# Kernel optimization log

Measured on AMD Instinct MI355X. Metric: run time of the kernel, lower is better.

## Reference

```python
import jax, jax.numpy as jnp
import numpy as np

B, N, D, S = 4, 8, 64, 8192  # batch, heads, dim_head, seq_len


def setup_inputs() -> dict:
    key = jax.random.key(0)
    kq, kk, kv = jax.random.split(key, 3)
    q = jax.random.normal(kq, (B, N, D, S), dtype=jnp.float32)
    k = jax.random.normal(kk, (B, N, D, S), dtype=jnp.float32)
    v = jax.random.normal(kv, (B, N, D, S), dtype=jnp.float32)
    return {"q": q, "k": k, "v": v}


def reference(q, k, v):
    # q, k, v: [b, n, d, s] = [batch, heads, dim_head, seq]
    scale = q.shape[-2] ** -0.5  # dim_head^-0.5
    qs = jax.nn.softmax(q, axis=-2) * scale   # softmax over feature dim
    ks = jax.nn.softmax(k, axis=-1)           # softmax over seq dim
    # kv context: [b, n, d, d] -- avoids the O(s^2) score matrix
    context = jnp.einsum('bnis,bnjs->bnij', ks, v)
    # out: [b, n, d, s]
    return jnp.einsum('bnij,bnis->bnjs', context, qs)
```

## Files before the change

kernel.cpp:

```cpp
#include <hip/hip_runtime.h>
#include <math.h>


constexpr int BHEADS = 32;
constexpr int DH     = 64;
constexpr int SEQ    = 8192;
constexpr float QSCALE = 0.125f;

__global__ __launch_bounds__(256)
void ctx_kernel(const float* __restrict__ K, const float* __restrict__ V,
                float* __restrict__ ctx, float* __restrict__ Z)
{
    const int head  = blockIdx.y;
    const int chunk = blockIdx.x;
    const int t     = threadIdx.x;

    const float* kh = K + (size_t)head * DH * SEQ;
    const float* vh = V + (size_t)head * DH * SEQ;

    __shared__ __align__(16) float et[64 * 64];
    __shared__ __align__(16) float vt[64 * 64];

    const int ti  = t >> 4;
    const int tj  = t & 15;
    const int s_l = t & 63;
    const int g   = t >> 6;

    float acc[4][4];
    #pragma unroll
    for (int a = 0; a < 4; ++a)
        #pragma unroll
        for (int b = 0; b < 4; ++b) acc[a][b] = 0.0f;
    float zacc[4] = {0.f, 0.f, 0.f, 0.f};

    for (int st = 0; st < 4; ++st) {
        const int s_base = chunk * 256 + st * 64;
        #pragma unroll
        for (int p = 0; p < 4; ++p) {
            const int c  = g + 4 * p;
            const int i0 = 4 * c;
            const size_t col = (size_t)s_base + s_l;
            float4 e4, v4;
            e4.x = __expf(kh[(size_t)(i0 + 0) * SEQ + col]);
            e4.y = __expf(kh[(size_t)(i0 + 1) * SEQ + col]);
            e4.z = __expf(kh[(size_t)(i0 + 2) * SEQ + col]);
            e4.w = __expf(kh[(size_t)(i0 + 3) * SEQ + col]);
            v4.x = vh[(size_t)(i0 + 0) * SEQ + col];
            v4.y = vh[(size_t)(i0 + 1) * SEQ + col];
            v4.z = vh[(size_t)(i0 + 2) * SEQ + col];
            v4.w = vh[(size_t)(i0 + 3) * SEQ + col];
            const int pos = c ^ (s_l & 15);
            ((float4*)(et + s_l * 64))[pos] = e4;
            ((float4*)(vt + s_l * 64))[pos] = v4;
        }
        __syncthreads();
        #pragma unroll 4
        for (int s = 0; s < 64; ++s) {
            const float4 e4 = ((const float4*)(et + s * 64))[ti ^ (s & 15)];
            const float4 v4 = ((const float4*)(vt + s * 64))[tj ^ (s & 15)];
            const float ee[4] = {e4.x, e4.y, e4.z, e4.w};
            const float vv[4] = {v4.x, v4.y, v4.z, v4.w};
            #pragma unroll
            for (int a = 0; a < 4; ++a) {
                #pragma unroll
                for (int b = 0; b < 4; ++b)
                    acc[a][b] = fmaf(ee[a], vv[b], acc[a][b]);
            }
            zacc[0] += ee[0]; zacc[1] += ee[1];
            zacc[2] += ee[2]; zacc[3] += ee[3];
        }
        __syncthreads();
    }

    float* ch = ctx + head * DH * DH;
    #pragma unroll
    for (int a = 0; a < 4; ++a)
        #pragma unroll
        for (int b = 0; b < 4; ++b)
            unsafeAtomicAdd(&ch[(4 * ti + a) * DH + 4 * tj + b], acc[a][b]);
    if (tj == 0) {
        #pragma unroll
        for (int a = 0; a < 4; ++a)
            unsafeAtomicAdd(&Z[head * DH + 4 * ti + a], zacc[a]);
    }
}

__global__ __launch_bounds__(256)
void out_kernel(const float* __restrict__ Q, const float* __restrict__ ctx,
                const float* __restrict__ Z, float* __restrict__ out)
{
    const int head  = blockIdx.y;
    const int stile = blockIdx.x;
    const int t     = threadIdx.x;
    const int s0    = stile * 128;

    __shared__ __align__(16) float eq[64 * 128];
    __shared__ __align__(16) float cs[64 * 64];
    __shared__ float rz[64];
    __shared__ float wpart[2][128];
    __shared__ __align__(16) float wsh[128];

    const float* qh = Q + (size_t)head * DH * SEQ + s0;

    if (t < 64) rz[t] = 1.0f / Z[head * DH + t];

    {
        const int i  = t >> 4;
        const int sg = t & 15;
        #pragma unroll
        for (int p = 0; p < 4; ++p) {
            const int row = i + 16 * p;
            #pragma unroll
            for (int h = 0; h < 2; ++h) {
                const int col = 4 * sg + 64 * h;
                float4 qv = *(const float4*)(qh + (size_t)row * SEQ + col);
                float4 ev;
                ev.x = __expf(qv.x); ev.y = __expf(qv.y);
                ev.z = __expf(qv.z); ev.w = __expf(qv.w);
                *(float4*)(eq + row * 128 + col) = ev;
            }
        }
    }
    __syncthreads();

    {
        const int i  = t >> 2;
        const int jg = t & 3;
        const float* ch = ctx + head * DH * DH;
        const float r = rz[i];
        #pragma unroll
        for (int p = 0; p < 4; ++p) {
            const int j0 = 4 * (jg + 4 * p);
            float4 cv = *(const float4*)(ch + i * DH + j0);
            cv.x *= r; cv.y *= r; cv.z *= r; cv.w *= r;
            *(float4*)(cs + i * DH + j0) = cv;
        }
    }
    {
        const int s = t & 127;
        const int h = t >> 7;
        float w = 0.0f;
        #pragma unroll 8
        for (int i = 32 * h; i < 32 * h + 32; ++i) w += eq[i * 128 + s];
        wpart[h][s] = w;
    }
    __syncthreads();
    if (t < 128) wsh[t] = QSCALE / (wpart[0][t] + wpart[1][t]);
    __syncthreads();

    const int tj = t >> 4;
    const int ts = t & 15;
    float acca[4][4], accb[4][4];
    #pragma unroll
    for (int a = 0; a < 4; ++a)
        #pragma unroll
        for (int b = 0; b < 4; ++b) { acca[a][b] = 0.f; accb[a][b] = 0.f; }

    #pragma unroll 4
    for (int i = 0; i < 64; ++i) {
        const float4 c4 = *(const float4*)(cs + i * DH + 4 * tj);
        const float4 a4 = *(const float4*)(eq + i * 128 + 4 * ts);
        const float4 b4 = *(const float4*)(eq + i * 128 + 64 + 4 * ts);
        const float cc[4] = {c4.x, c4.y, c4.z, c4.w};
        const float aa[4] = {a4.x, a4.y, a4.z, a4.w};
        const float bb[4] = {b4.x, b4.y, b4.z, b4.w};
        #pragma unroll
        for (int j = 0; j < 4; ++j) {
            #pragma unroll
            for (int x = 0; x < 4; ++x) {
                acca[j][x] = fmaf(cc[j], aa[x], acca[j][x]);
                accb[j][x] = fmaf(cc[j], bb[x], accb[j][x]);
            }
        }
    }

    const float4 wa = *(const float4*)(wsh + 4 * ts);
    const float4 wb = *(const float4*)(wsh + 64 + 4 * ts);
    float* oh = out + (size_t)head * DH * SEQ + s0;
    #pragma unroll
    for (int j = 0; j < 4; ++j) {
        const int row = 4 * tj + j;
        float4 o1, o2;
        o1.x = acca[j][0] * wa.x; o1.y = acca[j][1] * wa.y;
        o1.z = acca[j][2] * wa.z; o1.w = acca[j][3] * wa.w;
        o2.x = accb[j][0] * wb.x; o2.y = accb[j][1] * wb.y;
        o2.z = accb[j][2] * wb.z; o2.w = accb[j][3] * wb.w;
        *(float4*)(oh + (size_t)row * SEQ + 4 * ts) = o1;
        *(float4*)(oh + (size_t)row * SEQ + 64 + 4 * ts) = o2;
    }
}

extern "C" void kernel_launch(void* const* d_in, const int* in_sizes, int n_in,
                              void* d_out, int out_size, void* d_ws, size_t ws_size,
                              hipStream_t stream)
{
    const float* q = (const float*)d_in[0];
    const float* k = (const float*)d_in[1];
    const float* v = (const float*)d_in[2];
    float* out = (float*)d_out;

    float* ctx = (float*)d_ws;
    float* Z   = ctx + BHEADS * DH * DH;

    const size_t zero_bytes = (size_t)(BHEADS * DH * DH + BHEADS * DH) * sizeof(float);
    hipMemsetAsync(d_ws, 0, zero_bytes, stream);

    ctx_kernel<<<dim3(32, BHEADS), 256, 0, stream>>>(k, v, ctx, Z);
    out_kernel<<<dim3(64, BHEADS), 256, 0, stream>>>(q, ctx, Z, out);
}
```

Measured before the change: 272.4 us.

## Use fp16 MFMA for both context and output GEMMs with register prefetch

Both kernels replace their scalar FP32 FMA outer-product loops with 16x16x32 fp16 MFMA instructions. Exponentiated K, V, Q and the normalised context are converted to half precision in LDS. Global loads become float4 and are prefetched into registers for the next 64-column tile, overlapping memory with compute. The output kernel now handles 256 sequence columns per block in four sub-tiles with half the grid, and Z is reduced through shared memory before the atomics. The fp16 conversion trades accuracy for throughput, so exp values and V in half precision may lose precision.

```diff
diff --git a/kernel.cpp b/kernel.cpp
--- a/kernel.cpp
+++ b/kernel.cpp
@@ -1,6 +1,10 @@
 #include <hip/hip_runtime.h>
 #include <math.h>
 
+
+typedef _Float16 half8 __attribute__((ext_vector_type(8)));
+typedef _Float16 half4v __attribute__((ext_vector_type(4)));
+typedef float floatx4 __attribute__((ext_vector_type(4)));
 
 constexpr int BHEADS = 32;
 constexpr int DH     = 64;
@@ -14,74 +18,87 @@
     const int head  = blockIdx.y;
     const int chunk = blockIdx.x;
     const int t     = threadIdx.x;
+    const int lane  = t & 63;
+    const int w     = t >> 6;
+    const int ln    = lane & 15;
+    const int q8    = lane >> 4;
 
     const float* kh = K + (size_t)head * DH * SEQ;
     const float* vh = V + (size_t)head * DH * SEQ;
 
-    __shared__ __align__(16) float et[64 * 64];
-    __shared__ __align__(16) float vt[64 * 64];
-
-    const int ti  = t >> 4;
-    const int tj  = t & 15;
-    const int s_l = t & 63;
-    const int g   = t >> 6;
-
-    float acc[4][4];
-    #pragma unroll
-    for (int a = 0; a < 4; ++a)
-        #pragma unroll
-        for (int b = 0; b < 4; ++b) acc[a][b] = 0.0f;
+    __shared__ __align__(16) _Float16 et[64 * 72];
+    __shared__ __align__(16) _Float16 vt[64 * 72];
+    __shared__ float zred[64 * 16];
+
+    const int r0 = t >> 4;
+    const int sc = 4 * (t & 15);
+    const int s_blk = chunk * 256;
+
+    float4 pk[4], pv[4];
+    #pragma unroll
+    for (int p = 0; p < 4; ++p) {
+        const size_t off = (size_t)(r0 + 16 * p) * SEQ + s_blk + sc;
+        pk[p] = *(const float4*)(kh + off);
+        pv[p] = *(const float4*)(vh + off);
+    }
+
+    floatx4 acc[4];
+    #pragma unroll
+    for (int jt = 0; jt < 4; ++jt) acc[jt] = (floatx4){0.f, 0.f, 0.f, 0.f};
     float zacc[4] = {0.f, 0.f, 0.f, 0.f};
 
-    for (int st = 0; st < 4; ++st) {
-        const int s_base = chunk * 256 + st * 64;
+    for (int ts = 0; ts < 4; ++ts) {
         #pragma unroll
         for (int p = 0; p < 4; ++p) {
-            const int c  = g + 4 * p;
-            const int i0 = 4 * c;
-            const size_t col = (size_t)s_base + s_l;
-            float4 e4, v4;
-            e4.x = __expf(kh[(size_t)(i0 + 0) * SEQ + col]);
-            e4.y = __expf(kh[(size_t)(i0 + 1) * SEQ + col]);
-            e4.z = __expf(kh[(size_t)(i0 + 2) * SEQ + col]);
-            e4.w = __expf(kh[(size_t)(i0 + 3) * SEQ + col]);
-            v4.x = vh[(size_t)(i0 + 0) * SEQ + col];
-            v4.y = vh[(size_t)(i0 + 1) * SEQ + col];
-            v4.z = vh[(size_t)(i0 + 2) * SEQ + col];
-            v4.w = vh[(size_t)(i0 + 3) * SEQ + col];
-            const int pos = c ^ (s_l & 15);
-            ((float4*)(et + s_l * 64))[pos] = e4;
-            ((float4*)(vt + s_l * 64))[pos] = v4;
-        }
-        __syncthreads();
-        #pragma unroll 4
-        for (int s = 0; s < 64; ++s) {
-            const float4 e4 = ((const float4*)(et + s * 64))[ti ^ (s & 15)];
-            const float4 v4 = ((const float4*)(vt + s * 64))[tj ^ (s & 15)];
-            const float ee[4] = {e4.x, e4.y, e4.z, e4.w};
-            const float vv[4] = {v4.x, v4.y, v4.z, v4.w};
-            #pragma unroll
-            for (int a = 0; a < 4; ++a) {
-                #pragma unroll
-                for (int b = 0; b < 4; ++b)
-                    acc[a][b] = fmaf(ee[a], vv[b], acc[a][b]);
-            }
-            zacc[0] += ee[0]; zacc[1] += ee[1];
-            zacc[2] += ee[2]; zacc[3] += ee[3];
+            const int i = r0 + 16 * p;
+            const float e0 = __expf(pk[p].x), e1 = __expf(pk[p].y);
+            const float e2 = __expf(pk[p].z), e3 = __expf(pk[p].w);
+            zacc[p] += e0 + e1 + e2 + e3;
+            *(half4v*)(et + i * 72 + sc) =
+                (half4v){(_Float16)e0, (_Float16)e1, (_Float16)e2, (_Float16)e3};
+            *(half4v*)(vt + i * 72 + sc) =
+                (half4v){(_Float16)pv[p].x, (_Float16)pv[p].y,
+                         (_Float16)pv[p].z, (_Float16)pv[p].w};
+        }
+        __syncthreads();
+        if (ts < 3) {
+            #pragma unroll
+            for (int p = 0; p < 4; ++p) {
+                const size_t off = (size_t)(r0 + 16 * p) * SEQ + s_blk + (ts + 1) * 64 + sc;
+                pk[p] = *(const float4*)(kh + off);
+                pv[p] = *(const float4*)(vh + off);
+            }
+        }
+        #pragma unroll
+        for (int st = 0; st < 2; ++st) {
+            const half8 a = *(const half8*)(et + (16 * w + ln) * 72 + st * 32 + q8 * 8);
+            #pragma unroll
+            for (int jt = 0; jt < 4; ++jt) {
+                const half8 b = *(const half8*)(vt + (16 * jt + ln) * 72 + st * 32 + q8 * 8);
+                acc[jt] = __builtin_amdgcn_mfma_f32_16x16x32_f16(a, b, acc[jt], 0, 0, 0);
+            }
         }
         __syncthreads();
     }
 
     float* ch = ctx + head * DH * DH;
     #pragma unroll
-    for (int a = 0; a < 4; ++a)
-        #pragma unroll
-        for (int b = 0; b < 4; ++b)
-            unsafeAtomicAdd(&ch[(4 * ti + a) * DH + 4 * tj + b], acc[a][b]);
-    if (tj == 0) {
-        #pragma unroll
-        for (int a = 0; a < 4; ++a)
-            unsafeAtomicAdd(&Z[head * DH + 4 * ti + a], zacc[a]);
+    for (int jt = 0; jt < 4; ++jt) {
+        #pragma unroll
+        for (int rr = 0; rr < 4; ++rr) {
+            const int i = 16 * w + q8 * 4 + rr;
+            const int j = 16 * jt + ln;
+            unsafeAtomicAdd(&ch[i * DH + j], acc[jt][rr]);
+        }
+    }
+    #pragma unroll
+    for (int p = 0; p < 4; ++p) zred[(r0 + 16 * p) * 16 + (t & 15)] = zacc[p];
+    __syncthreads();
+    if (t < 64) {
+        float z = 0.f;
+        #pragma unroll
+        for (int c = 0; c < 16; ++c) z += zred[t * 16 + c];
+        unsafeAtomicAdd(&Z[head * DH + t], z);
     }
 }
 
@@ -89,104 +106,107 @@
 void out_kernel(const float* __restrict__ Q, const float* __restrict__ ctx,
                 const float* __restrict__ Z, float* __restrict__ out)
 {
-    const int head  = blockIdx.y;
-    const int stile = blockIdx.x;
-    const int t     = threadIdx.x;
-    const int s0    = stile * 128;
-
-    __shared__ __align__(16) float eq[64 * 128];
-    __shared__ __align__(16) float cs[64 * 64];
-    __shared__ float rz[64];
-    __shared__ float wpart[2][128];
-    __shared__ __align__(16) float wsh[128];
-
-    const float* qh = Q + (size_t)head * DH * SEQ + s0;
-
-    if (t < 64) rz[t] = 1.0f / Z[head * DH + t];
+    const int head = blockIdx.y;
+    const int sb   = blockIdx.x;
+    const int t    = threadIdx.x;
+    const int lane = t & 63;
+    const int w    = t >> 6;
+    const int ln   = lane & 15;
+    const int q8   = lane >> 4;
+
+    __shared__ __align__(16) _Float16 czT[64 * 72];
+    __shared__ __align__(16) float    qf[64 * 68];
+    __shared__ __align__(16) _Float16 eqT[64 * 64];
+    __shared__ float wred[64 * 4];
+    __shared__ float rwsh[64];
+
+    const float* qh = Q + (size_t)head * DH * SEQ;
+    const int r0 = t >> 4;
+    const int sc = 4 * (t & 15);
+    const int s0 = sb * 256;
+
+    float4 pq[4];
+    #pragma unroll
+    for (int p = 0; p < 4; ++p)
+        pq[p] = *(const float4*)(qh + (size_t)(r0 + 16 * p) * SEQ + s0 + sc);
 
     {
-        const int i  = t >> 4;
-        const int sg = t & 15;
+        const float* ch = ctx + head * DH * DH;
         #pragma unroll
         for (int p = 0; p < 4; ++p) {
-            const int row = i + 16 * p;
+            const int i = r0 + 16 * p;
+            const float rz = 1.0f / Z[head * DH + i];
+            const float4 c4 = *(const float4*)(ch + i * DH + sc);
+            czT[(sc + 0) * 72 + i] = (_Float16)(c4.x * rz);
+            czT[(sc + 1) * 72 + i] = (_Float16)(c4.y * rz);
+            czT[(sc + 2) * 72 + i] = (_Float16)(c4.z * rz);
+            czT[(sc + 3) * 72 + i] = (_Float16)(c4.w * rz);
+        }
+    }
+    __syncthreads();
+
+    const half8 a0 = *(const half8*)(czT + (16 * w + ln) * 72 + 0 + q8 * 8);
+    const half8 a1 = *(const half8*)(czT + (16 * w + ln) * 72 + 32 + q8 * 8);
+
+    for (int r = 0; r < 4; ++r) {
+        #pragma unroll
+        for (int p = 0; p < 4; ++p)
+            *(float4*)(qf + (r0 + 16 * p) * 68 + sc) = pq[p];
+        __syncthreads();
+        {
+            const int s  = t & 63;
+            const int cg = t >> 6;
+            float wsum = 0.f;
             #pragma unroll
             for (int h = 0; h < 2; ++h) {
-                const int col = 4 * sg + 64 * h;
-                float4 qv = *(const float4*)(qh + (size_t)row * SEQ + col);
-                float4 ev;
-                ev.x = __expf(qv.x); ev.y = __expf(qv.y);
-                ev.z = __expf(qv.z); ev.w = __expf(qv.w);
-                *(float4*)(eq + row * 128 + col) = ev;
-            }
-        }
-    }
-    __syncthreads();
-
-    {
-        const int i  = t >> 2;
-        const int jg = t & 3;
-        const float* ch = ctx + head * DH * DH;
-        const float r = rz[i];
-        #pragma unroll
-        for (int p = 0; p < 4; ++p) {
-            const int j0 = 4 * (jg + 4 * p);
-            float4 cv = *(const float4*)(ch + i * DH + j0);
-            cv.x *= r; cv.y *= r; cv.z *= r; cv.w *= r;
-            *(float4*)(cs + i * DH + j0) = cv;
-        }
-    }
-    {
-        const int s = t & 127;
-        const int h = t >> 7;
-        float w = 0.0f;
-        #pragma unroll 8
-        for (int i = 32 * h; i < 32 * h + 32; ++i) w += eq[i * 128 + s];
-        wpart[h][s] = w;
-    }
-    __syncthreads();
-    if (t < 128) wsh[t] = QSCALE / (wpart[0][t] + wpart[1][t]);
-    __syncthreads();
-
-    const int tj = t >> 4;
-    const int ts = t & 15;
-    float acca[4][4], accb[4][4];
-    #pragma unroll
-    for (int a = 0; a < 4; ++a)
-        #pragma unroll
-        for (int b = 0; b < 4; ++b) { acca[a][b] = 0.f; accb[a][b] = 0.f; }
-
-    #pragma unroll 4
-    for (int i = 0; i < 64; ++i) {
-        const float4 c4 = *(const float4*)(cs + i * DH + 4 * tj);
-        const float4 a4 = *(const float4*)(eq + i * 128 + 4 * ts);
-        const float4 b4 = *(const float4*)(eq + i * 128 + 64 + 4 * ts);
-        const float cc[4] = {c4.x, c4.y, c4.z, c4.w};
-        const float aa[4] = {a4.x, a4.y, a4.z, a4.w};
-        const float bb[4] = {b4.x, b4.y, b4.z, b4.w};
-        #pragma unroll
-        for (int j = 0; j < 4; ++j) {
-            #pragma unroll
-            for (int x = 0; x < 4; ++x) {
-                acca[j][x] = fmaf(cc[j], aa[x], acca[j][x]);
-                accb[j][x] = fmaf(cc[j], bb[x], accb[j][x]);
-            }
-        }
-    }
-
-    const float4 wa = *(const float4*)(wsh + 4 * ts);
-    const float4 wb = *(const float4*)(wsh + 64 + 4 * ts);
-    float* oh = out + (size_t)head * DH * SEQ + s0;
-    #pragma unroll
-    for (int j = 0; j < 4; ++j) {
-        const int row = 4 * tj + j;
-        float4 o1, o2;
-        o1.x = acca[j][0] * wa.x; o1.y = acca[j][1] * wa.y;
-        o1.z = acca[j][2] * wa.z; o1.w = acca[j][3] * wa.w;
-        o2.x = accb[j][0] * wb.x; o2.y = accb[j][1] * wb.y;
-        o2.z = accb[j][2] * wb.z; o2.w = accb[j][3] * wb.w;
-        *(float4*)(oh + (size_t)row * SEQ + 4 * ts) = o1;
-        *(float4*)(oh + (size_t)row * SEQ + 64 + 4 * ts) = o2;
+                const int cc = cg + 4 * h;
+                half8 pk8;
+                #pragma unroll
+                for (int jj = 0; jj < 8; ++jj) {
+                    const float e = __expf(qf[(8 * cc + jj) * 68 + s]);
+                    wsum += e;
+                    pk8[jj] = (_Float16)e;
+                }
+                *(half8*)(eqT + s * 64 + ((cc ^ (s & 7)) * 8)) = pk8;
+            }
+            wred[s * 4 + cg] = wsum;
+        }
+        __syncthreads();
+        if (r < 3) {
+            #pragma unroll
+            for (int p = 0; p < 4; ++p)
+                pq[p] = *(const float4*)(qh + (size_t)(r0 + 16 * p) * SEQ
+                                         + s0 + (r + 1) * 64 + sc);
+        }
+        if (t < 64)
+            rwsh[t] = QSCALE / (wred[t * 4] + wred[t * 4 + 1]
+                                + wred[t * 4 + 2] + wred[t * 4 + 3]);
+        floatx4 acc[4];
+        #pragma unroll
+        for (int nt = 0; nt < 4; ++nt) acc[nt] = (floatx4){0.f, 0.f, 0.f, 0.f};
+        #pragma unroll
+        for (int st = 0; st < 2; ++st) {
+            const half8 a = (st == 0) ? a0 : a1;
+            #pragma unroll
+            for (int nt = 0; nt < 4; ++nt) {
+                const int s  = 16 * nt + ln;
+                const int cc = st * 4 + q8;
+                const half8 b = *(const half8*)(eqT + s * 64 + ((cc ^ (s & 7)) * 8));
+                acc[nt] = __builtin_amdgcn_mfma_f32_16x16x32_f16(a, b, acc[nt], 0, 0, 0);
+            }
+        }
+        __syncthreads();
+        float* oh = out + (size_t)head * DH * SEQ + s0 + r * 64;
+        #pragma unroll
+        for (int nt = 0; nt < 4; ++nt) {
+            const int s = 16 * nt + ln;
+            const float rw = rwsh[s];
+            #pragma unroll
+            for (int rr = 0; rr < 4; ++rr) {
+                const int j = 16 * w + q8 * 4 + rr;
+                oh[(size_t)j * SEQ + s] = acc[nt][rr] * rw;
+            }
+        }
     }
 }
 
@@ -206,5 +226,5 @@
     hipMemsetAsync(d_ws, 0, zero_bytes, stream);
 
     ctx_kernel<<<dim3(32, BHEADS), 256, 0, stream>>>(k, v, ctx, Z);
-    out_kernel<<<dim3(64, BHEADS), 256, 0, stream>>>(q, ctx, Z, out);
+    out_kernel<<<dim3(32, BHEADS), 256, 0, stream>>>(q, ctx, Z, out);
 }
```

Measured after the change: 238.1 us. 1.14x faster.
